# Performance work log

Measured on AMD Instinct MI355X. Metric: run time of the kernel, lower is better.

## Reference

```python
import jax, jax.numpy as jnp
import numpy as np

# Dimensions
B, C, H, W = 16, 256, 32, 32
CO, DK, DV, NH = 256, 128, 128, 8   # channels_out, depth_k, depth_v, num_heads
KS = 3                              # conv kernel size
DKH, DVH = DK // NH, DV // NH


def setup_inputs() -> dict:
    key = jax.random.key(0)
    ks = jax.random.split(key, 4)
    s = 0.05
    return {
        "x": jax.random.normal(ks[0], (B, C, H, W), jnp.float32),
        # conv branch: 3x3 conv -> channels_out - depth_v = 128, HWIO layout
        "conv_w": jax.random.normal(ks[1], (KS, KS, C, CO - DV), jnp.float32) * s,
        "conv_b": jnp.zeros((CO - DV,), jnp.float32),
        # 1x1 QKV conv: 2*depth_k + depth_v output channels
        "qkv_w": jax.random.normal(ks[2], (2 * DK + DV, C), jnp.float32) * s,
        "qkv_b": jnp.zeros((2 * DK + DV,), jnp.float32),
        # 1x1 output projection conv: depth_v -> depth_v
        "proj_w": jax.random.normal(ks[3], (DV, DV), jnp.float32) * s,
        "proj_b": jnp.zeros((DV,), jnp.float32),
    }


def reference(x, conv_w, conv_b, qkv_w, qkv_b, proj_w, proj_b):
    # --- conv branch (3x3, SAME padding, NCHW) ---
    conv_out = jax.lax.conv_general_dilated(
        x, conv_w, window_strides=(1, 1), padding='SAME',
        dimension_numbers=('NCHW', 'HWIO', 'NCHW'))
    conv_out = conv_out + conv_b[None, :, None, None]

    # --- attention branch ---
    # 1x1 conv == channel matmul
    kqv = jnp.einsum('bchw,oc->bohw', x, qkv_w) + qkv_b[None, :, None, None]
    # tf.split order: k, q, v
    k, q, v = jnp.split(kqv, [DK, 2 * DK], axis=1)
    q = q * (DKH ** -0.5)

    def heads(t, d):  # (B, NH*d, H, W) -> (B, NH, H*W, d)
        return t.reshape(B, NH, d, H * W).transpose(0, 1, 3, 2)

    qh, kh, vh = heads(q, DKH), heads(k, DKH), heads(v, DVH)
    logits = jnp.einsum('bnqd,bnkd->bnqk', qh, kh)          # (B,NH,HW,HW)
    weights = jax.nn.softmax(logits, axis=-1)
    attn = jnp.einsum('bnqk,bnkd->bnqd', weights, vh)       # (B,NH,HW,DVH)
    # combine heads, head-major channel order -> (B, DV, H, W)
    attn = attn.transpose(0, 1, 3, 2).reshape(B, DV, H, W)
    attn_out = jnp.einsum('bchw,oc->bohw', attn, proj_w) + proj_b[None, :, None, None]

    return jnp.concatenate([conv_out, attn_out], axis=1)
```

## Files before the change

### kernel.cpp

```cpp
#include <hip/hip_runtime.h>
#include <hip/hip_bf16.h>


#define Bn   16
#define Cin  256
#define HWp  1024
#define COn  256
#define NHn  8

typedef short short8  __attribute__((ext_vector_type(8)));
typedef short short4v __attribute__((ext_vector_type(4)));
typedef float f32x4   __attribute__((ext_vector_type(4)));
typedef float f32x16  __attribute__((ext_vector_type(16)));

__device__ inline short bf16_rne(float f) {
  unsigned u = __builtin_bit_cast(unsigned, f);
  u += 0x7fffu + ((u >> 16) & 1u);
  return (short)(u >> 16);
}

__device__ inline unsigned pkbf(float a, float b) {
  __hip_bfloat162 h = __float22bfloat162_rn(make_float2(a, b));
  unsigned u;
  __builtin_memcpy(&u, &h, 4);
  return u;
}

__device__ inline void store_bf8(short* dst, const float* f) {
  uint4 u;
  u.x = pkbf(f[0], f[1]); u.y = pkbf(f[2], f[3]);
  u.z = pkbf(f[4], f[5]); u.w = pkbf(f[6], f[7]);
  *(uint4*)dst = u;
}

__global__ __launch_bounds__(256) void prep_all(
    const float* __restrict__ cw, const float* __restrict__ qw,
    const float* __restrict__ pw, short* __restrict__ wfc,
    short* __restrict__ wfq, short* __restrict__ wfp)
{
  const int gid  = blockIdx.x * 256 + threadIdx.x;
  const int lane = gid & 63, frag = gid >> 6;
  const int l15 = lane & 15, q = lane >> 4;
  short8 pk;
  if (frag < 576) {
    const int cf = frag & 7, cq = (frag >> 3) & 7, kk = frag >> 6;
    const int co = cf * 16 + l15, c = cq * 32 + q * 8;
#pragma unroll
    for (int j = 0; j < 8; ++j)
      pk[j] = bf16_rne(cw[(size_t)(kk * Cin + c + j) * 128 + co]);
    *(short8*)(wfc + (size_t)frag * 512 + lane * 8) = pk;
  } else if (frag < 768) {
    const int f = frag - 576;
    const int rt = f >> 3, kf = f & 7;
    const int o = rt * 16 + l15, c = kf * 32 + q * 8;
#pragma unroll
    for (int j = 0; j < 8; ++j) pk[j] = bf16_rne(qw[o * Cin + c + j]);
    *(short8*)(wfq + (size_t)f * 512 + lane * 8) = pk;
  } else if (frag < 800) {
    const int f = frag - 768;
    const int rt = f >> 2, kf = f & 3;
    const int o = rt * 16 + l15, c = kf * 32 + q * 8;
#pragma unroll
    for (int j = 0; j < 8; ++j) pk[j] = bf16_rne(pw[o * 128 + c + j]);
    *(short8*)(wfp + (size_t)f * 512 + lane * 8) = pk;
  }
}

__global__ __launch_bounds__(256) void prep_x(
    const float* __restrict__ x, short* __restrict__ xt)
{
  __shared__ short t[32][262];
  const int tid = threadIdx.x;
  const int hw0 = (blockIdx.x & 3) * 256;
  const int c0  = ((blockIdx.x >> 2) & 7) * 32;
  const int b   = blockIdx.x >> 5;

#pragma unroll 4
  for (int cc = 0; cc < 32; ++cc)
    t[cc][tid] = bf16_rne(x[(size_t)(b * Cin + c0 + cc) * HWp + hw0 + tid]);
  __syncthreads();

  for (int s = tid; s < 1024; s += 256) {
    const int hwl = s >> 2, q4 = s & 3;
    short8 pk;
#pragma unroll
    for (int j = 0; j < 8; ++j) pk[j] = t[q4 * 8 + j][hwl];
    *(short8*)&xt[((size_t)(b * HWp + hw0 + hwl)) * 256 + c0 + q4 * 8] = pk;
  }
}

__global__ __launch_bounds__(512) void conv_mfma(
    const short* __restrict__ xt, const short* __restrict__ wf,
    const float* __restrict__ bias, float* __restrict__ out)
{
  __shared__ short xl[2][5712];
  const int tid  = threadIdx.x;
  const int lane = tid & 63, wv = tid >> 6;
  const int l15  = lane & 15, g = lane >> 4;
  const int b  = blockIdx.x >> 4;
  const int h0 = (blockIdx.x & 15) * 2;

  f32x4 acc[4] = {};

#define STAGE(chunk)                                                          \
  {                                                                           \
    const int c0_ = (chunk) * 32;                                             \
    short* dst_ = xl[(chunk) & 1];                                            \
    for (int s = tid; s < 544; s += 512) {                                    \
      const int cell = s >> 2, qq = s & 3;                                    \
      const int r = cell / 34, col = cell - r * 34;                           \
      const int h_in = h0 - 1 + r, w_in = col - 1;                            \
      short8 v = {};                                                          \
      if (h_in >= 0 && h_in < 32 && w_in >= 0 && w_in < 32)                   \
        v = *(const short8*)&xt[((size_t)(b * HWp + h_in * 32 + w_in)) * 256  \
                                + c0_ + qq * 8];                              \
      *(short8*)&dst_[cell * 42 + qq * 8] = v;                                \
    }                                                                         \
  }

  STAGE(0);
  __syncthreads();

  for (int cq = 0; cq < 8; ++cq) {
    if (cq < 7) STAGE(cq + 1);
    const short* cur = xl[cq & 1];
#pragma unroll
    for (int kk = 0; kk < 9; ++kk) {
      const int kh = kk / 3, kw = kk - kh * 3;
      const short8 a0 = *(const short8*)(wf + (size_t)((kk * 8 + cq) * 8 + wv) * 512 + lane * 8);
#pragma unroll
      for (int bf = 0; bf < 4; ++bf) {
        const int m = bf * 16 + l15;
        const int r = (m >> 5) + kh, col = (m & 31) + kw;
        const short8 xv = *(const short8*)&cur[(r * 34 + col) * 42 + g * 8];
        acc[bf] = __builtin_amdgcn_mfma_f32_16x16x32_bf16(a0, xv, acc[bf], 0, 0, 0);
      }
    }
    __syncthreads();
  }
#undef STAGE

  const int cob = wv * 16 + g * 4;
#pragma unroll
  for (int r = 0; r < 4; ++r) {
    const int co = cob + r;
    const float bv = bias[co];
    float* op = out + (size_t)(b * COn + co) * HWp + h0 * 32 + l15;
#pragma unroll
    for (int bf = 0; bf < 4; ++bf)
      op[bf * 16] = acc[bf][r] + bv;
  }
}

__global__ __launch_bounds__(512) void qkv_mfma(
    const short* __restrict__ xt, const short* __restrict__ wfq,
    const float* __restrict__ bias, short* __restrict__ qbuf,
    short* __restrict__ kbuf, short* __restrict__ vtbuf)
{
  __shared__ short xl[16384];
  const int tid = threadIdx.x, lane = tid & 63, wv = tid >> 6;
  const int l15 = lane & 15, g = lane >> 4;
  const int hw0 = blockIdx.x * 64;
  const int b   = blockIdx.y;

  {
    const int qq = tid & 3, kf = (tid >> 2) & 7, hl = tid >> 5;
#pragma unroll
    for (int mt = 0; mt < 4; ++mt) {
      const int p  = ((mt * 8 + kf) * 4 + qq) * 16 + hl;
      const int sw = p ^ ((p >> 4) & 7);
      const short8 v = *(const short8*)&xt[((size_t)(b * HWp + hw0 + mt * 16 + hl)) * 256
                                           + kf * 32 + qq * 8];
      *(short8*)&xl[sw * 8] = v;
    }
  }
  __syncthreads();

  f32x4 acc[3][4] = {};
  for (int kf = 0; kf < 8; ++kf) {
    short8 bfr[4];
#pragma unroll
    for (int mt = 0; mt < 4; ++mt) {
      const int q  = ((mt * 8 + kf) * 4 + g) * 16 + l15;
      const int sw = q ^ ((q >> 4) & 7);
      bfr[mt] = *(const short8*)&xl[sw * 8];
    }
#pragma unroll
    for (int i = 0; i < 3; ++i) {
      const int rt = wv * 3 + i;
      const short8 af = *(const short8*)(wfq + ((size_t)(rt * 8 + kf) * 64 + lane) * 8);
#pragma unroll
      for (int mt = 0; mt < 4; ++mt)
        acc[i][mt] = __builtin_amdgcn_mfma_f32_16x16x32_bf16(af, bfr[mt], acc[i][mt], 0, 0, 0);
    }
  }

#pragma unroll
  for (int i = 0; i < 3; ++i) {
    const int rt = wv * 3 + i;
    float bv[4];
#pragma unroll
    for (int r = 0; r < 4; ++r) bv[r] = bias[rt * 16 + 4 * g + r];
    if (rt < 8) {
      short* kp = kbuf + ((size_t)(b * NHn + rt) * HWp + hw0) * 16 + 4 * g;
#pragma unroll
      for (int mt = 0; mt < 4; ++mt) {
        short4v s;
#pragma unroll
        for (int r = 0; r < 4; ++r) s[r] = bf16_rne(acc[i][mt][r] + bv[r]);
        *(short4v*)(kp + (size_t)(mt * 16 + l15) * 16) = s;
      }
    } else if (rt < 16) {
      short* qp = qbuf + ((size_t)(b * NHn + rt - 8) * HWp + hw0) * 16 + 4 * g;
#pragma unroll
      for (int mt = 0; mt < 4; ++mt) {
        short4v s;
#pragma unroll
        for (int r = 0; r < 4; ++r) s[r] = bf16_rne((acc[i][mt][r] + bv[r]) * 0.25f);
        *(short4v*)(qp + (size_t)(mt * 16 + l15) * 16) = s;
      }
    } else {
      short* vp = vtbuf + (size_t)(b * NHn + rt - 16) * 16 * HWp;
#pragma unroll
      for (int mt = 0; mt < 4; ++mt)
#pragma unroll
        for (int r = 0; r < 4; ++r)
          vp[(size_t)(4 * g + r) * HWp + hw0 + mt * 16 + l15] =
              bf16_rne(acc[i][mt][r] + bv[r]);
    }
  }
}

__global__ __launch_bounds__(256) void attn_mfma(
    const short* __restrict__ qb, const short* __restrict__ kb,
    const short* __restrict__ vt, float* __restrict__ abuf)
{
  __shared__ short P[4][2][32][40];
  const int tid = threadIdx.x, lane = tid & 63, wv = tid >> 6;
  const int l15 = lane & 15, g = lane >> 4;
  const int l31 = lane & 31, hi = lane >> 5;
  const int h = blockIdx.y, b = blockIdx.z, bh = b * NHn + h;
  const int q0 = blockIdx.x * 128 + wv * 32;

  const short* qp = qb + (size_t)bh * HWp * 16;
  const short* kp = kb + (size_t)bh * HWp * 16;
  const short* vp = vt + (size_t)bh * 16 * HWp;

  const short8 qf = *(const short8*)(qp + (size_t)(q0 + l31) * 16 + hi * 8);

  f32x4 o0 = {}, o1 = {};
  float lsum = 0.f;

  for (int kt = 0; kt < HWp; kt += 64) {
#pragma unroll
    for (int t = 0; t < 2; ++t) {
      const int k0 = kt + t * 32;
      const short8 kf = *(const short8*)(kp + (size_t)(k0 + l31) * 16 + hi * 8);
      f32x16 z = {};
      const f32x16 s = __builtin_amdgcn_mfma_f32_32x32x16_bf16(kf, qf, z, 0, 0, 0);
      float p[16];
#pragma unroll
      for (int r = 0; r < 16; ++r) { p[r] = __expf(s[r]); lsum += p[r]; }
#pragma unroll
      for (int rg = 0; rg < 4; ++rg) {
        uint2 u;
        u.x = pkbf(p[4 * rg + 0], p[4 * rg + 1]);
        u.y = pkbf(p[4 * rg + 2], p[4 * rg + 3]);
        *(uint2*)&P[wv][t][l31][8 * rg + 4 * hi] = u;
      }
      const short8 vf = *(const short8*)(vp + (size_t)l15 * HWp + k0 + g * 8);
      const short8 pf0 = *(const short8*)&P[wv][t][l15][g * 8];
      o0 = __builtin_amdgcn_mfma_f32_16x16x32_bf16(vf, pf0, o0, 0, 0, 0);
      const short8 pf1 = *(const short8*)&P[wv][t][16 + l15][g * 8];
      o1 = __builtin_amdgcn_mfma_f32_16x16x32_bf16(vf, pf1, o1, 0, 0, 0);
    }
  }

  const float l  = lsum + __shfl_xor(lsum, 32);
  const float li0 = 1.f / __shfl(l, l15);
  const float li1 = 1.f / __shfl(l, 16 + l15);
#pragma unroll
  for (int r = 0; r < 4; ++r) {
    const int d = 4 * g + r;
    float* op = abuf + (size_t)(b * 128 + h * 16 + d) * HWp + q0;
    op[l15]      = o0[r] * li0;
    op[16 + l15] = o1[r] * li1;
  }
}

__global__ __launch_bounds__(256) void proj_mfma(
    const float* __restrict__ a, const short* __restrict__ wfp,
    const float* __restrict__ bias, float* __restrict__ out)
{
  __shared__ short xl[8192];
  const int tid = threadIdx.x, lane = tid & 63, wv = tid >> 6;
  const int l15 = lane & 15, g = lane >> 4;
  const int hw0 = blockIdx.x * 64;
  const int b   = blockIdx.y;

#pragma unroll
  for (int it = 0; it < 4; ++it) {
    const int p  = it * 256 + tid;
    const int mt = p >> 8, kf = (p >> 6) & 3, qq = (p >> 4) & 3, hl = p & 15;
    const float* ap = a + (size_t)(b * 128 + kf * 32 + qq * 8) * HWp
                        + hw0 + mt * 16 + hl;
    float fv[8];
#pragma unroll
    for (int j = 0; j < 8; ++j) fv[j] = ap[(size_t)j * HWp];
    store_bf8(&xl[p * 8], fv);
  }
  __syncthreads();

  f32x4 acc[2][4] = {};
  for (int kf = 0; kf < 4; ++kf) {
    short8 bfr[4];
#pragma unroll
    for (int mt = 0; mt < 4; ++mt)
      bfr[mt] = *(const short8*)&xl[(((mt * 4 + kf) * 4 + g) * 16 + l15) * 8];
#pragma unroll
    for (int i = 0; i < 2; ++i) {
      const int rt = wv * 2 + i;
      const short8 af = *(const short8*)(wfp + ((size_t)(rt * 4 + kf) * 64 + lane) * 8);
#pragma unroll
      for (int mt = 0; mt < 4; ++mt)
        acc[i][mt] = __builtin_amdgcn_mfma_f32_16x16x32_bf16(af, bfr[mt], acc[i][mt], 0, 0, 0);
    }
  }

#pragma unroll
  for (int i = 0; i < 2; ++i) {
    const int rt = wv * 2 + i;
#pragma unroll
    for (int r = 0; r < 4; ++r) {
      const int o = rt * 16 + 4 * g + r;
      const float bv = bias[o];
      float* op = out + (size_t)(b * COn + 128 + o) * HWp + hw0 + l15;
#pragma unroll
      for (int mt = 0; mt < 4; ++mt)
        op[mt * 16] = acc[i][mt][r] + bv;
    }
  }
}

extern "C" void kernel_launch(void* const* d_in, const int* in_sizes, int n_in,
                              void* d_out, int out_size, void* d_ws, size_t ws_size,
                              hipStream_t stream) {
  const float* x      = (const float*)d_in[0];
  const float* conv_w = (const float*)d_in[1];
  const float* conv_b = (const float*)d_in[2];
  const float* qkv_w  = (const float*)d_in[3];
  const float* qkv_b  = (const float*)d_in[4];
  const float* proj_w = (const float*)d_in[5];
  const float* proj_b = (const float*)d_in[6];
  float* out = (float*)d_out;

  char* wsb = (char*)d_ws;
  short* wfc    = (short*)wsb;
  short* wfq    = (short*)(wsb + (1u << 20));
  short* wfp    = (short*)(wsb + (2u << 20));
  short* qbuf16 = (short*)(wsb + (8u << 20));
  short* kbuf16 = (short*)(wsb + (12u << 20));
  short* vtbuf  = (short*)(wsb + (16u << 20));
  float* abuf   = (float*)(wsb + (20u << 20));
  short* xtbuf  = (short*)(wsb + (28u << 20));

  prep_all  <<<dim3(200), 256, 0, stream>>>(conv_w, qkv_w, proj_w, wfc, wfq, wfp);
  prep_x    <<<dim3(512), 256, 0, stream>>>(x, xtbuf);
  conv_mfma <<<dim3(256), 512, 0, stream>>>(xtbuf, wfc, conv_b, out);
  qkv_mfma  <<<dim3(16, 16), 512, 0, stream>>>(xtbuf, wfq, qkv_b, qbuf16, kbuf16, vtbuf);
  attn_mfma <<<dim3(8, 8, 16), 256, 0, stream>>>(qbuf16, kbuf16, vtbuf, abuf);
  proj_mfma <<<dim3(16, 16), 256, 0, stream>>>(abuf, wfp, proj_b, out);
}
```

Baseline: 182.5 us.

## Fuse prep kernels and retile conv with register-staged double buffering

Merges the weight-packing and x-transpose prep kernels into a single launch that branches on block index. The 3x3 conv kernel is retiled to one output row per 256-thread block (512 blocks instead of 256). Each wave now computes 2 output-channel fragments by 2 spatial fragments, so weight fragments are reused across spatial positions. The next input chunk is loaded into registers before the MFMA loop and written to LDS after it, overlapping global loads with compute. In exchange, neighbouring rows reload more halo data and the extra staging registers may lower occupancy.

```diff
diff --git a/kernel.cpp b/kernel.cpp
--- a/kernel.cpp
+++ b/kernel.cpp
@@ -33,123 +33,139 @@
   *(uint4*)dst = u;
 }
 
-__global__ __launch_bounds__(256) void prep_all(
+__global__ __launch_bounds__(256) void prep_fused(
     const float* __restrict__ cw, const float* __restrict__ qw,
-    const float* __restrict__ pw, short* __restrict__ wfc,
-    short* __restrict__ wfq, short* __restrict__ wfp)
-{
-  const int gid  = blockIdx.x * 256 + threadIdx.x;
-  const int lane = gid & 63, frag = gid >> 6;
-  const int l15 = lane & 15, q = lane >> 4;
-  short8 pk;
-  if (frag < 576) {
-    const int cf = frag & 7, cq = (frag >> 3) & 7, kk = frag >> 6;
-    const int co = cf * 16 + l15, c = cq * 32 + q * 8;
-#pragma unroll
-    for (int j = 0; j < 8; ++j)
-      pk[j] = bf16_rne(cw[(size_t)(kk * Cin + c + j) * 128 + co]);
-    *(short8*)(wfc + (size_t)frag * 512 + lane * 8) = pk;
-  } else if (frag < 768) {
-    const int f = frag - 576;
-    const int rt = f >> 3, kf = f & 7;
-    const int o = rt * 16 + l15, c = kf * 32 + q * 8;
-#pragma unroll
-    for (int j = 0; j < 8; ++j) pk[j] = bf16_rne(qw[o * Cin + c + j]);
-    *(short8*)(wfq + (size_t)f * 512 + lane * 8) = pk;
-  } else if (frag < 800) {
-    const int f = frag - 768;
-    const int rt = f >> 2, kf = f & 3;
-    const int o = rt * 16 + l15, c = kf * 32 + q * 8;
-#pragma unroll
-    for (int j = 0; j < 8; ++j) pk[j] = bf16_rne(pw[o * 128 + c + j]);
-    *(short8*)(wfp + (size_t)f * 512 + lane * 8) = pk;
-  }
-}
-
-__global__ __launch_bounds__(256) void prep_x(
-    const float* __restrict__ x, short* __restrict__ xt)
+    const float* __restrict__ pw, const float* __restrict__ x,
+    short* __restrict__ wfc, short* __restrict__ wfq,
+    short* __restrict__ wfp, short* __restrict__ xt)
 {
   __shared__ short t[32][262];
   const int tid = threadIdx.x;
-  const int hw0 = (blockIdx.x & 3) * 256;
-  const int c0  = ((blockIdx.x >> 2) & 7) * 32;
-  const int b   = blockIdx.x >> 5;
-
+  if (blockIdx.x < 200) {
+    const int gid  = blockIdx.x * 256 + tid;
+    const int lane = gid & 63, frag = gid >> 6;
+    const int l15 = lane & 15, q = lane >> 4;
+    short8 pk;
+    if (frag < 576) {
+      const int cf = frag & 7, cq = (frag >> 3) & 7, kk = frag >> 6;
+      const int co = cf * 16 + l15, c = cq * 32 + q * 8;
+#pragma unroll
+      for (int j = 0; j < 8; ++j)
+        pk[j] = bf16_rne(cw[(size_t)(kk * Cin + c + j) * 128 + co]);
+      *(short8*)(wfc + (size_t)frag * 512 + lane * 8) = pk;
+    } else if (frag < 768) {
+      const int f = frag - 576;
+      const int rt = f >> 3, kf = f & 7;
+      const int o = rt * 16 + l15, c = kf * 32 + q * 8;
+#pragma unroll
+      for (int j = 0; j < 8; ++j) pk[j] = bf16_rne(qw[o * Cin + c + j]);
+      *(short8*)(wfq + (size_t)f * 512 + lane * 8) = pk;
+    } else if (frag < 800) {
+      const int f = frag - 768;
+      const int rt = f >> 2, kf = f & 3;
+      const int o = rt * 16 + l15, c = kf * 32 + q * 8;
+#pragma unroll
+      for (int j = 0; j < 8; ++j) pk[j] = bf16_rne(pw[o * 128 + c + j]);
+      *(short8*)(wfp + (size_t)f * 512 + lane * 8) = pk;
+    }
+  } else {
+    const int bid = blockIdx.x - 200;
+    const int hw0 = (bid & 3) * 256;
+    const int c0  = ((bid >> 2) & 7) * 32;
+    const int b   = bid >> 5;
 #pragma unroll 4
-  for (int cc = 0; cc < 32; ++cc)
-    t[cc][tid] = bf16_rne(x[(size_t)(b * Cin + c0 + cc) * HWp + hw0 + tid]);
-  __syncthreads();
-
-  for (int s = tid; s < 1024; s += 256) {
-    const int hwl = s >> 2, q4 = s & 3;
-    short8 pk;
-#pragma unroll
-    for (int j = 0; j < 8; ++j) pk[j] = t[q4 * 8 + j][hwl];
-    *(short8*)&xt[((size_t)(b * HWp + hw0 + hwl)) * 256 + c0 + q4 * 8] = pk;
-  }
-}
-
-__global__ __launch_bounds__(512) void conv_mfma(
+    for (int cc = 0; cc < 32; ++cc)
+      t[cc][tid] = bf16_rne(x[(size_t)(b * Cin + c0 + cc) * HWp + hw0 + tid]);
+    __syncthreads();
+    for (int s = tid; s < 1024; s += 256) {
+      const int hwl = s >> 2, q4 = s & 3;
+      short8 pk;
+#pragma unroll
+      for (int j = 0; j < 8; ++j) pk[j] = t[q4 * 8 + j][hwl];
+      *(short8*)&xt[((size_t)(b * HWp + hw0 + hwl)) * 256 + c0 + q4 * 8] = pk;
+    }
+  }
+}
+
+__global__ __launch_bounds__(256) void conv_mfma(
     const short* __restrict__ xt, const short* __restrict__ wf,
     const float* __restrict__ bias, float* __restrict__ out)
 {
-  __shared__ short xl[2][5712];
+  __shared__ short xl[2][102 * 42];
   const int tid  = threadIdx.x;
   const int lane = tid & 63, wv = tid >> 6;
   const int l15  = lane & 15, g = lane >> 4;
-  const int b  = blockIdx.x >> 4;
-  const int h0 = (blockIdx.x & 15) * 2;
-
-  f32x4 acc[4] = {};
-
-#define STAGE(chunk)                                                          \
+  const int b  = blockIdx.x >> 5;
+  const int h0 = blockIdx.x & 31;
+
+  f32x4 acc[2][2] = {};
+  short8 rv[2];
+
+#define LOADC(c0_)                                                            \
   {                                                                           \
-    const int c0_ = (chunk) * 32;                                             \
-    short* dst_ = xl[(chunk) & 1];                                            \
-    for (int s = tid; s < 544; s += 512) {                                    \
-      const int cell = s >> 2, qq = s & 3;                                    \
-      const int r = cell / 34, col = cell - r * 34;                           \
-      const int h_in = h0 - 1 + r, w_in = col - 1;                            \
-      short8 v = {};                                                          \
-      if (h_in >= 0 && h_in < 32 && w_in >= 0 && w_in < 32)                   \
-        v = *(const short8*)&xt[((size_t)(b * HWp + h_in * 32 + w_in)) * 256  \
-                                + c0_ + qq * 8];                              \
-      *(short8*)&dst_[cell * 42 + qq * 8] = v;                                \
+    _Pragma("unroll")                                                         \
+    for (int i = 0; i < 2; ++i) {                                             \
+      const int s = tid + i * 256;                                            \
+      if (s < 408) {                                                          \
+        const int cell = s >> 2, qq = s & 3;                                  \
+        const int r = cell / 34, col = cell - r * 34;                         \
+        const int h_in = h0 - 1 + r, w_in = col - 1;                          \
+        short8 v = {};                                                        \
+        if (h_in >= 0 && h_in < 32 && w_in >= 0 && w_in < 32)                 \
+          v = *(const short8*)&xt[((size_t)(b * HWp + h_in * 32 + w_in)) * 256\
+                                  + (c0_) + qq * 8];                          \
+        rv[i] = v;                                                            \
+      }                                                                       \
     }                                                                         \
   }
-
-  STAGE(0);
+#define WRITEC(bi_)                                                           \
+  {                                                                           \
+    _Pragma("unroll")                                                         \
+    for (int i = 0; i < 2; ++i) {                                             \
+      const int s = tid + i * 256;                                            \
+      if (s < 408) {                                                          \
+        const int cell = s >> 2, qq = s & 3;                                  \
+        *(short8*)&xl[bi_][cell * 42 + qq * 8] = rv[i];                       \
+      }                                                                       \
+    }                                                                         \
+  }
+
+  LOADC(0); WRITEC(0);
   __syncthreads();
 
   for (int cq = 0; cq < 8; ++cq) {
-    if (cq < 7) STAGE(cq + 1);
+    if (cq < 7) LOADC((cq + 1) * 32);
     const short* cur = xl[cq & 1];
 #pragma unroll
     for (int kk = 0; kk < 9; ++kk) {
       const int kh = kk / 3, kw = kk - kh * 3;
-      const short8 a0 = *(const short8*)(wf + (size_t)((kk * 8 + cq) * 8 + wv) * 512 + lane * 8);
-#pragma unroll
-      for (int bf = 0; bf < 4; ++bf) {
-        const int m = bf * 16 + l15;
-        const int r = (m >> 5) + kh, col = (m & 31) + kw;
-        const short8 xv = *(const short8*)&cur[(r * 34 + col) * 42 + g * 8];
-        acc[bf] = __builtin_amdgcn_mfma_f32_16x16x32_bf16(a0, xv, acc[bf], 0, 0, 0);
+#pragma unroll
+      for (int af = 0; af < 2; ++af) {
+        const short8 a0 = *(const short8*)(wf + (size_t)((kk * 8 + cq) * 8 + wv * 2 + af) * 512 + lane * 8);
+#pragma unroll
+        for (int bf = 0; bf < 2; ++bf) {
+          const int m = bf * 16 + l15;
+          const short8 xv = *(const short8*)&cur[(kh * 34 + m + kw) * 42 + g * 8];
+          acc[af][bf] = __builtin_amdgcn_mfma_f32_16x16x32_bf16(a0, xv, acc[af][bf], 0, 0, 0);
+        }
       }
     }
+    if (cq < 7) WRITEC((cq + 1) & 1);
     __syncthreads();
   }
-#undef STAGE
-
-  const int cob = wv * 16 + g * 4;
-#pragma unroll
-  for (int r = 0; r < 4; ++r) {
-    const int co = cob + r;
-    const float bv = bias[co];
-    float* op = out + (size_t)(b * COn + co) * HWp + h0 * 32 + l15;
-#pragma unroll
-    for (int bf = 0; bf < 4; ++bf)
-      op[bf * 16] = acc[bf][r] + bv;
-  }
+#undef LOADC
+#undef WRITEC
+
+#pragma unroll
+  for (int af = 0; af < 2; ++af)
+#pragma unroll
+    for (int r = 0; r < 4; ++r) {
+      const int co = (wv * 2 + af) * 16 + 4 * g + r;
+      const float bv = bias[co];
+      float* op = out + (size_t)(b * COn + co) * HWp + h0 * 32 + l15;
+      op[0]  = acc[af][0][r] + bv;
+      op[16] = acc[af][1][r] + bv;
+    }
 }
 
 __global__ __launch_bounds__(512) void qkv_mfma(
@@ -364,9 +380,9 @@
   float* abuf   = (float*)(wsb + (20u << 20));
   short* xtbuf  = (short*)(wsb + (28u << 20));
 
-  prep_all  <<<dim3(200), 256, 0, stream>>>(conv_w, qkv_w, proj_w, wfc, wfq, wfp);
-  prep_x    <<<dim3(512), 256, 0, stream>>>(x, xtbuf);
-  conv_mfma <<<dim3(256), 512, 0, stream>>>(xtbuf, wfc, conv_b, out);
+  prep_fused<<<dim3(712), 256, 0, stream>>>(conv_w, qkv_w, proj_w, x,
+                                            wfc, wfq, wfp, xtbuf);
+  conv_mfma <<<dim3(512), 256, 0, stream>>>(xtbuf, wfc, conv_b, out);
   qkv_mfma  <<<dim3(16, 16), 512, 0, stream>>>(xtbuf, wfq, qkv_b, qbuf16, kbuf16, vtbuf);
   attn_mfma <<<dim3(8, 8, 16), 256, 0, stream>>>(qbuf16, kbuf16, vtbuf, abuf);
   proj_mfma <<<dim3(16, 16), 256, 0, stream>>>(abuf, wfp, proj_b, out);
```

After: 169.9 us. 6.9% less time.
